# Kernel tuning notes

Hardware: AMD Instinct MI355X
Metric: run time of the kernel (lower is better)

## Reference

```python
import jax, jax.numpy as jnp
import numpy as np

N_NODES = 50000
N_EDGES = 800000
D_IN, D_HID, D_OUT = 64, 128, 64


def _glorot(key, fan_in, fan_out):
    lim = (6.0 / (fan_in + fan_out)) ** 0.5
    return jax.random.uniform(key, (fan_in, fan_out), jnp.float32, -lim, lim)


def setup_inputs() -> dict:
    key = jax.random.key(0)
    ks = jax.random.split(key, 10)
    x = jax.random.normal(ks[0], (N_NODES, D_IN), jnp.float32)
    edge_index = jax.random.randint(ks[1], (2, N_EDGES), 0, N_NODES, jnp.int64)
    # GINConv1 MLP: Linear(D_IN->D_HID), ReLU, Linear(D_HID->D_HID)
    W1a = _glorot(ks[2], D_IN, D_HID); b1a = jnp.zeros((D_HID,), jnp.float32)
    W1b = _glorot(ks[3], D_HID, D_HID); b1b = jnp.zeros((D_HID,), jnp.float32)
    # GINConv2 MLP: Linear(D_HID->D_HID), ReLU, Linear(D_HID->D_OUT)
    W2a = _glorot(ks[4], D_HID, D_HID); b2a = jnp.zeros((D_HID,), jnp.float32)
    W2b = _glorot(ks[5], D_HID, D_OUT); b2b = jnp.zeros((D_OUT,), jnp.float32)
    return {"x": x, "edge_index": edge_index,
            "W1a": W1a, "b1a": b1a, "W1b": W1b, "b1b": b1b,
            "W2a": W2a, "b2a": b2a, "W2b": W2b, "b2b": b2b}


def _gin_conv(x, src, dst, Wa, ba, Wb, bb):
    # GIN aggregation (eps = 0): h_i = x_i + sum_{j in N(i)} x_j
    msgs = x[src]                                   # [E, d] gather
    agg = jax.ops.segment_sum(msgs, dst, num_segments=x.shape[0])  # [N, d]
    h = x + agg
    # 2-layer MLP
    h = jax.nn.relu(h @ Wa + ba)
    return h @ Wb + bb


def reference(x, edge_index, W1a, b1a, W1b, b1b, W2a, b2a, W2b, b2b):
    src, dst = edge_index[0], edge_index[1]
    h = jax.nn.relu(_gin_conv(x, src, dst, W1a, b1a, W1b, b1b))
    h = jax.nn.relu(_gin_conv(h, src, dst, W2a, b2a, W2b, b2b))
    return h
```

## Files before the change

kernel.cpp:

```cpp
#include <hip/hip_runtime.h>

#define N_NODES 50000
#define N_EDGES 800000

typedef __attribute__((ext_vector_type(8))) short short8;
typedef __attribute__((ext_vector_type(4))) float floatx4;

static __device__ __forceinline__ unsigned short f2b(float f) {
    unsigned int u = __float_as_uint(f);
    unsigned int r = u + 0x7fffu + ((u >> 16) & 1u);
    return (unsigned short)(r >> 16);
}
static __device__ __forceinline__ unsigned int pk(float a, float b) {
    return (unsigned)f2b(a) | ((unsigned)f2b(b) << 16);
}
static __device__ __forceinline__ float blo(unsigned int u) {
    return __uint_as_float(u << 16);
}
static __device__ __forceinline__ float bhi(unsigned int u) {
    return __uint_as_float(u & 0xffff0000u);
}

static __device__ __forceinline__ void acc4(float* f, uint4 v0, uint4 v1,
                                            uint4 v2, uint4 v3) {
    f[0] += (blo(v0.x) + blo(v1.x)) + (blo(v2.x) + blo(v3.x));
    f[1] += (bhi(v0.x) + bhi(v1.x)) + (bhi(v2.x) + bhi(v3.x));
    f[2] += (blo(v0.y) + blo(v1.y)) + (blo(v2.y) + blo(v3.y));
    f[3] += (bhi(v0.y) + bhi(v1.y)) + (bhi(v2.y) + bhi(v3.y));
    f[4] += (blo(v0.z) + blo(v1.z)) + (blo(v2.z) + blo(v3.z));
    f[5] += (bhi(v0.z) + bhi(v1.z)) + (bhi(v2.z) + bhi(v3.z));
    f[6] += (blo(v0.w) + blo(v1.w)) + (blo(v2.w) + blo(v3.w));
    f[7] += (bhi(v0.w) + bhi(v1.w)) + (bhi(v2.w) + bhi(v3.w));
}

__global__ void hist_rank_kernel(const int* __restrict__ dst,
                                 int* __restrict__ deg, int* __restrict__ rank,
                                 int n) {
    int i = blockIdx.x * blockDim.x + threadIdx.x;
    if (i < n) rank[i] = atomicAdd(&deg[dst[i]], 1);
}

__global__ __launch_bounds__(1024) void scanA_kernel(
    const int* __restrict__ deg, int* __restrict__ bsum, int n) {
    __shared__ int s[1024];
    const int tid = threadIdx.x;
    int i = blockIdx.x * 1024 + tid;
    s[tid] = (i < n) ? ((deg[i] + 3) & ~3) : 0;
    __syncthreads();
    for (int d = 512; d > 0; d >>= 1) {
        if (tid < d) s[tid] += s[tid + d];
        __syncthreads();
    }
    if (tid == 0) bsum[blockIdx.x] = s[0];
}

__global__ __launch_bounds__(1024) void scanC_kernel(
    const int* __restrict__ deg, const int* __restrict__ bsum,
    int* __restrict__ off, int n) {
    __shared__ int s[1024];
    __shared__ int bpref;
    const int tid = threadIdx.x;
    if (tid == 0) {
        int p = 0;
        for (int j = 0; j < blockIdx.x; ++j) p += bsum[j];
        bpref = p;
    }
    const int i = blockIdx.x * 1024 + tid;
    const int v = (i < n) ? ((deg[i] + 3) & ~3) : 0;
    s[tid] = v;
    __syncthreads();
    for (int d = 1; d < 1024; d <<= 1) {
        int t = (tid >= d) ? s[tid - d] : 0;
        __syncthreads();
        s[tid] += t;
        __syncthreads();
    }
    const int excl = s[tid] - v + bpref;
    if (i < n) {
        off[i] = excl;
        if (i == n - 1) off[n] = excl + v;
    }
}

__global__ void fill_kernel(const int* __restrict__ src,
                            const int* __restrict__ dst,
                            const int* __restrict__ rank,
                            const int* __restrict__ off,
                            const int* __restrict__ deg,
                            unsigned short* __restrict__ nbr, int n,
                            int n_nodes) {
    int i = blockIdx.x * blockDim.x + threadIdx.x;
    if (i < n) {
        nbr[off[dst[i]] + rank[i]] = (unsigned short)src[i];
    } else if (i < n + n_nodes) {
        const int v = i - n;
        const int base = off[v];
        const int d = deg[v];
        const int pd = (d + 3) & ~3;
        for (int k = d; k < pd; ++k) nbr[base + k] = (unsigned short)N_NODES;
    }
}

__global__ __launch_bounds__(256) void prep_kernel(
    const float* __restrict__ W1a, const float* __restrict__ W1b,
    const float* __restrict__ W2a, const float* __restrict__ W2b,
    const float* __restrict__ x, unsigned short* __restrict__ W1aT,
    unsigned short* __restrict__ W1bT, unsigned short* __restrict__ W2aT,
    unsigned short* __restrict__ W2bT, unsigned short* __restrict__ xb,
    unsigned short* __restrict__ h, int* __restrict__ deg) {
    int i = blockIdx.x * 256 + threadIdx.x;
    if (i < 8192) {
        int n = i >> 6, k = i & 63;
        W1aT[i] = f2b(W1a[k * 128 + n]);
    } else if (i < 24576) {
        int j = i - 8192, n = j >> 7, k = j & 127;
        W1bT[j] = f2b(W1b[k * 128 + n]);
    } else if (i < 40960) {
        int j = i - 24576, n = j >> 7, k = j & 127;
        W2aT[j] = f2b(W2a[k * 128 + n]);
    } else if (i < 49152) {
        int j = i - 40960, n = j >> 7, k = j & 127;
        W2bT[j] = f2b(W2b[k * 64 + n]);
    } else if (i < 49152 + N_NODES * 16) {
        int j = i - 49152;
        float4 v = ((const float4*)x)[j];
        uint2 o;
        o.x = pk(v.x, v.y);
        o.y = pk(v.z, v.w);
        ((uint2*)xb)[j] = o;
    } else if (i < 49152 + N_NODES * 16 + N_NODES) {
        int j = i - (49152 + N_NODES * 16);
        deg[j] = 0;
    } else {
        int j = i - (49152 + N_NODES * 16 + N_NODES);
        uint4 z = {0u, 0u, 0u, 0u};
        if (j < 8)
            ((uint4*)(xb + (size_t)N_NODES * 64))[j] = z;
        else if (j < 24)
            ((uint4*)(h + (size_t)N_NODES * 128))[j - 8] = z;
    }
}

template <int DIN, int DH, int DOUT, bool OUT_BF16>
__global__ __launch_bounds__(256) void gin_fused_kernel(
    const unsigned short* __restrict__ xin, const int* __restrict__ off,
    const unsigned short* __restrict__ nbr,
    const unsigned short* __restrict__ WaT, const float* __restrict__ ba,
    const unsigned short* __restrict__ WbT, const float* __restrict__ bb,
    void* __restrict__ outp, int n_rows) {
    constexpr int LPR = DIN / 8;
    constexpr int ROWS = 256 / LPR;
    constexpr int SA = DIN + 16;
    constexpr int SH = DH + 16;
    __shared__ __attribute__((aligned(16))) unsigned short tA[ROWS * SA];
    __shared__ __attribute__((aligned(16))) unsigned short hidA[ROWS * SH];

    const int tid = threadIdx.x;
    const int row0 = blockIdx.x * ROWS;
    const int grp = tid / LPR;
    const int c = tid % LPR;
    const int node = row0 + grp;

    float f[8] = {0.f, 0.f, 0.f, 0.f, 0.f, 0.f, 0.f, 0.f};
    const uint4* xr = (const uint4*)xin;
    if (node < n_rows) {
        const uint4 a = xr[(size_t)node * LPR + c];
        f[0] = blo(a.x); f[1] = bhi(a.x);
        f[2] = blo(a.y); f[3] = bhi(a.y);
        f[4] = blo(a.z); f[5] = bhi(a.z);
        f[6] = blo(a.w); f[7] = bhi(a.w);
        const int lo = off[node], hi = off[node + 1];
        int j = lo;
        for (; j + 8 <= hi; j += 8) {
            const uint2 i0 = *(const uint2*)&nbr[j];
            const uint2 i1 = *(const uint2*)&nbr[j + 4];
            const int s0 = i0.x & 0xffff, s1 = i0.x >> 16;
            const int s2 = i0.y & 0xffff, s3 = i0.y >> 16;
            const int s4 = i1.x & 0xffff, s5 = i1.x >> 16;
            const int s6 = i1.y & 0xffff, s7 = i1.y >> 16;
            const uint4 v0 = xr[(size_t)s0 * LPR + c];
            const uint4 v1 = xr[(size_t)s1 * LPR + c];
            const uint4 v2 = xr[(size_t)s2 * LPR + c];
            const uint4 v3 = xr[(size_t)s3 * LPR + c];
            const uint4 v4 = xr[(size_t)s4 * LPR + c];
            const uint4 v5 = xr[(size_t)s5 * LPR + c];
            const uint4 v6 = xr[(size_t)s6 * LPR + c];
            const uint4 v7 = xr[(size_t)s7 * LPR + c];
            acc4(f, v0, v1, v2, v3);
            acc4(f, v4, v5, v6, v7);
        }
        if (j < hi) {
            const uint2 i0 = *(const uint2*)&nbr[j];
            const int s0 = i0.x & 0xffff, s1 = i0.x >> 16;
            const int s2 = i0.y & 0xffff, s3 = i0.y >> 16;
            const uint4 v0 = xr[(size_t)s0 * LPR + c];
            const uint4 v1 = xr[(size_t)s1 * LPR + c];
            const uint4 v2 = xr[(size_t)s2 * LPR + c];
            const uint4 v3 = xr[(size_t)s3 * LPR + c];
            acc4(f, v0, v1, v2, v3);
        }
    }
    uint4 o;
    o.x = pk(f[0], f[1]);
    o.y = pk(f[2], f[3]);
    o.z = pk(f[4], f[5]);
    o.w = pk(f[6], f[7]);
    *(uint4*)&tA[grp * SA + c * 8] = o;
    __syncthreads();

    constexpr int MT = ROWS / 16;
    constexpr int NSPLIT = 4 / MT;
    const int lane = tid & 63;
    const int wv = tid >> 6;
    const int wm = wv % MT;
    const int wn = wv / MT;
    const int quad = lane >> 4;
    const int l16 = lane & 15;
    const int m0 = wm * 16;

    short8 a1[DIN / 32];
#pragma unroll
    for (int kk = 0; kk < DIN / 32; ++kk)
        a1[kk] = *(const short8*)&tA[(m0 + l16) * SA + kk * 32 + quad * 8];
#pragma unroll
    for (int nt = 0; nt < DH / (16 * NSPLIT); ++nt) {
        const int col = wn * (DH / NSPLIT) + nt * 16 + l16;
        floatx4 acc = {0.f, 0.f, 0.f, 0.f};
#pragma unroll
        for (int kk = 0; kk < DIN / 32; ++kk) {
            short8 b = *(const short8*)&WaT[col * DIN + kk * 32 + quad * 8];
            acc = __builtin_amdgcn_mfma_f32_16x16x32_bf16(a1[kk], b, acc, 0, 0, 0);
        }
        const float bias = ba[col];
#pragma unroll
        for (int r = 0; r < 4; ++r) {
            const float v = fmaxf(acc[r] + bias, 0.f);
            hidA[(m0 + quad * 4 + r) * SH + col] = f2b(v);
        }
    }
    __syncthreads();

    short8 a2[DH / 32];
#pragma unroll
    for (int kk = 0; kk < DH / 32; ++kk)
        a2[kk] = *(const short8*)&hidA[(m0 + l16) * SH + kk * 32 + quad * 8];
#pragma unroll
    for (int nt = 0; nt < DOUT / (16 * NSPLIT); ++nt) {
        const int col = wn * (DOUT / NSPLIT) + nt * 16 + l16;
        floatx4 acc = {0.f, 0.f, 0.f, 0.f};
#pragma unroll
        for (int kk = 0; kk < DH / 32; ++kk) {
            short8 b = *(const short8*)&WbT[col * DH + kk * 32 + quad * 8];
            acc = __builtin_amdgcn_mfma_f32_16x16x32_bf16(a2[kk], b, acc, 0, 0, 0);
        }
        const float bias = bb[col];
#pragma unroll
        for (int r = 0; r < 4; ++r) {
            const float v = fmaxf(acc[r] + bias, 0.f);
            const int grow = row0 + m0 + quad * 4 + r;
            if (grow < n_rows) {
                if (OUT_BF16)
                    ((unsigned short*)outp)[(size_t)grow * DOUT + col] = f2b(v);
                else
                    ((float*)outp)[(size_t)grow * DOUT + col] = v;
            }
        }
    }
}

extern "C" void kernel_launch(void* const* d_in, const int* in_sizes, int n_in,
                              void* d_out, int out_size, void* d_ws,
                              size_t ws_size, hipStream_t stream) {
    const float* x   = (const float*)d_in[0];
    const int*   ei  = (const int*)d_in[1];
    const float* W1a = (const float*)d_in[2];
    const float* b1a = (const float*)d_in[3];
    const float* W1b = (const float*)d_in[4];
    const float* b1b = (const float*)d_in[5];
    const float* W2a = (const float*)d_in[6];
    const float* b2a = (const float*)d_in[7];
    const float* W2b = (const float*)d_in[8];
    const float* b2b = (const float*)d_in[9];
    float* out = (float*)d_out;

    const int* src = ei;
    const int* dst = ei + N_EDGES;

    unsigned short* xb = (unsigned short*)d_ws;
    unsigned short* h  = xb + (size_t)(N_NODES + 1) * 64;
    unsigned short* W1aT = h + (size_t)(N_NODES + 1) * 128;
    unsigned short* W1bT = W1aT + 8192;
    unsigned short* W2aT = W1bT + 16384;
    unsigned short* W2bT = W2aT + 16384;
    int* deg  = (int*)(W2bT + 8192);
    int* off  = deg + N_NODES;
    int* bsum = off + N_NODES + 1;
    int* rank = bsum + 64;
    unsigned short* nbr = (unsigned short*)(rank + N_EDGES);

    constexpr int NB = (N_NODES + 1023) / 1024;
    constexpr int PREP_THREADS = 49152 + N_NODES * 16 + N_NODES + 24;

    prep_kernel<<<(PREP_THREADS + 255) / 256, 256, 0, stream>>>(
        W1a, W1b, W2a, W2b, x, W1aT, W1bT, W2aT, W2bT, xb, h, deg);

    hist_rank_kernel<<<(N_EDGES + 255) / 256, 256, 0, stream>>>(dst, deg, rank,
                                                                N_EDGES);
    scanA_kernel<<<NB, 1024, 0, stream>>>(deg, bsum, N_NODES);
    scanC_kernel<<<NB, 1024, 0, stream>>>(deg, bsum, off, N_NODES);
    fill_kernel<<<(N_EDGES + N_NODES + 255) / 256, 256, 0, stream>>>(
        src, dst, rank, off, deg, nbr, N_EDGES, N_NODES);

    gin_fused_kernel<64, 128, 128, true>
        <<<(N_NODES + 31) / 32, 256, 0, stream>>>(xb, off, nbr, W1aT, b1a, W1bT,
                                                  b1b, h, N_NODES);

    gin_fused_kernel<128, 128, 64, false>
        <<<(N_NODES + 15) / 16, 256, 0, stream>>>(h, off, nbr, W2aT, b2a, W2bT,
                                                  b2b, out, N_NODES);
}
```

Before: 218.3 us.

## Sort nodes by in-degree so fused GIN blocks process balanced neighbor counts

Adds a degree histogram (an extra block in the scan-reduce kernel) and a counting-sort pass (extra blocks in the scan kernel) that builds a permutation of nodes ordered by clamped in-degree. Both fused GIN kernels then process rows in permuted order and scatter outputs back to the original node index. The aim is to cut intra-block and intra-wave load imbalance in the neighbor-gather loop. The cost is a serial single-block histogram, an extra indirection, scattered output writes, and less locality when reading each node's own row.

```diff
diff --git a/kernel.cpp b/kernel.cpp
--- a/kernel.cpp
+++ b/kernel.cpp
@@ -41,9 +41,34 @@
 }
 
 __global__ __launch_bounds__(1024) void scanA_kernel(
-    const int* __restrict__ deg, int* __restrict__ bsum, int n) {
+    const int* __restrict__ deg, int* __restrict__ bsum,
+    int* __restrict__ binoff, int n, int nb) {
+    const int tid = threadIdx.x;
+    if ((int)blockIdx.x == nb) {
+        __shared__ int bins[4][256];
+        ((int*)bins)[tid] = 0;
+        __syncthreads();
+        const int sub = (tid >> 6) & 3;
+        for (int i = tid; i < n; i += 1024) {
+            int d = deg[i];
+            d = d > 255 ? 255 : d;
+            atomicAdd(&bins[sub][d], 1);
+        }
+        __syncthreads();
+        if (tid < 256)
+            bins[0][tid] =
+                bins[0][tid] + bins[1][tid] + bins[2][tid] + bins[3][tid];
+        __syncthreads();
+        if (tid == 0) {
+            int run = 0;
+            for (int b = 0; b < 256; ++b) {
+                binoff[b] = run;
+                run += bins[0][b];
+            }
+        }
+        return;
+    }
     __shared__ int s[1024];
-    const int tid = threadIdx.x;
     int i = blockIdx.x * 1024 + tid;
     s[tid] = (i < n) ? ((deg[i] + 3) & ~3) : 0;
     __syncthreads();
@@ -56,13 +81,24 @@
 
 __global__ __launch_bounds__(1024) void scanC_kernel(
     const int* __restrict__ deg, const int* __restrict__ bsum,
-    int* __restrict__ off, int n) {
+    int* __restrict__ off, int* __restrict__ binoff, int* __restrict__ perm,
+    int n, int nb) {
+    const int tid = threadIdx.x;
+    if ((int)blockIdx.x >= nb) {
+        const int i = ((int)blockIdx.x - nb) * 1024 + tid;
+        if (i < n) {
+            int d = deg[i];
+            d = d > 255 ? 255 : d;
+            const int pos = atomicAdd(&binoff[d], 1);
+            perm[pos] = i;
+        }
+        return;
+    }
     __shared__ int s[1024];
     __shared__ int bpref;
-    const int tid = threadIdx.x;
     if (tid == 0) {
         int p = 0;
-        for (int j = 0; j < blockIdx.x; ++j) p += bsum[j];
+        for (int j = 0; j < (int)blockIdx.x; ++j) p += bsum[j];
         bpref = p;
     }
     const int i = blockIdx.x * 1024 + tid;
@@ -144,7 +180,7 @@
 template <int DIN, int DH, int DOUT, bool OUT_BF16>
 __global__ __launch_bounds__(256) void gin_fused_kernel(
     const unsigned short* __restrict__ xin, const int* __restrict__ off,
-    const unsigned short* __restrict__ nbr,
+    const unsigned short* __restrict__ nbr, const int* __restrict__ perm,
     const unsigned short* __restrict__ WaT, const float* __restrict__ ba,
     const unsigned short* __restrict__ WbT, const float* __restrict__ bb,
     void* __restrict__ outp, int n_rows) {
@@ -159,11 +195,12 @@
     const int row0 = blockIdx.x * ROWS;
     const int grp = tid / LPR;
     const int c = tid % LPR;
-    const int node = row0 + grp;
+    const int gnode = row0 + grp;
 
     float f[8] = {0.f, 0.f, 0.f, 0.f, 0.f, 0.f, 0.f, 0.f};
     const uint4* xr = (const uint4*)xin;
-    if (node < n_rows) {
+    if (gnode < n_rows) {
+        const int node = perm[gnode];
         const uint4 a = xr[(size_t)node * LPR + c];
         f[0] = blo(a.x); f[1] = bhi(a.x);
         f[2] = blo(a.y); f[3] = bhi(a.y);
@@ -257,12 +294,13 @@
 #pragma unroll
         for (int r = 0; r < 4; ++r) {
             const float v = fmaxf(acc[r] + bias, 0.f);
-            const int grow = row0 + m0 + quad * 4 + r;
-            if (grow < n_rows) {
+            const int gr = row0 + m0 + quad * 4 + r;
+            if (gr < n_rows) {
+                const int orow = perm[gr];
                 if (OUT_BF16)
-                    ((unsigned short*)outp)[(size_t)grow * DOUT + col] = f2b(v);
+                    ((unsigned short*)outp)[(size_t)orow * DOUT + col] = f2b(v);
                 else
-                    ((float*)outp)[(size_t)grow * DOUT + col] = v;
+                    ((float*)outp)[(size_t)orow * DOUT + col] = v;
             }
         }
     }
@@ -292,11 +330,13 @@
     unsigned short* W1bT = W1aT + 8192;
     unsigned short* W2aT = W1bT + 16384;
     unsigned short* W2bT = W2aT + 16384;
-    int* deg  = (int*)(W2bT + 8192);
-    int* off  = deg + N_NODES;
-    int* bsum = off + N_NODES + 1;
-    int* rank = bsum + 64;
-    unsigned short* nbr = (unsigned short*)(rank + N_EDGES);
+    int* deg    = (int*)(W2bT + 8192);
+    int* off    = deg + N_NODES;
+    int* bsum   = off + N_NODES + 1;
+    int* rank   = bsum + 64;
+    int* perm   = rank + N_EDGES;
+    int* binoff = perm + N_NODES;
+    unsigned short* nbr = (unsigned short*)(binoff + 256);
 
     constexpr int NB = (N_NODES + 1023) / 1024;
     constexpr int PREP_THREADS = 49152 + N_NODES * 16 + N_NODES + 24;
@@ -306,16 +346,17 @@
 
     hist_rank_kernel<<<(N_EDGES + 255) / 256, 256, 0, stream>>>(dst, deg, rank,
                                                                 N_EDGES);
-    scanA_kernel<<<NB, 1024, 0, stream>>>(deg, bsum, N_NODES);
-    scanC_kernel<<<NB, 1024, 0, stream>>>(deg, bsum, off, N_NODES);
+    scanA_kernel<<<NB + 1, 1024, 0, stream>>>(deg, bsum, binoff, N_NODES, NB);
+    scanC_kernel<<<2 * NB, 1024, 0, stream>>>(deg, bsum, off, binoff, perm,
+                                              N_NODES, NB);
     fill_kernel<<<(N_EDGES + N_NODES + 255) / 256, 256, 0, stream>>>(
         src, dst, rank, off, deg, nbr, N_EDGES, N_NODES);
 
     gin_fused_kernel<64, 128, 128, true>
-        <<<(N_NODES + 31) / 32, 256, 0, stream>>>(xb, off, nbr, W1aT, b1a, W1bT,
-                                                  b1b, h, N_NODES);
+        <<<(N_NODES + 31) / 32, 256, 0, stream>>>(xb, off, nbr, perm, W1aT, b1a,
+                                                  W1bT, b1b, h, N_NODES);
 
     gin_fused_kernel<128, 128, 64, false>
-        <<<(N_NODES + 15) / 16, 256, 0, stream>>>(h, off, nbr, W2aT, b2a, W2bT,
-                                                  b2b, out, N_NODES);
-}
+        <<<(N_NODES + 15) / 16, 256, 0, stream>>>(h, off, nbr, perm, W2aT, b2a,
+                                                  W2bT, b2b, out, N_NODES);
+}
```

Result: slower. 345.4 us (+58.2%).

## Sort rows by degree within block and unroll neighbor gather by 16

Applied to the files above, without the earlier changes.

Each block computes node degrees, ranks them in shared memory and assigns rows to thread groups in degree order, so lanes in the same wavefront handle nodes of similar degree and diverge less. Results are written back to their original row slot in shared memory. The main gather loop is unrolled to 16 neighbors per iteration to keep more loads in flight. This adds a small ranking pass with extra syncs and raises register pressure.

```diff
diff --git a/kernel.cpp b/kernel.cpp
--- a/kernel.cpp
+++ b/kernel.cpp
@@ -62,7 +62,7 @@
     const int tid = threadIdx.x;
     if (tid == 0) {
         int p = 0;
-        for (int j = 0; j < blockIdx.x; ++j) p += bsum[j];
+        for (int j = 0; j < (int)blockIdx.x; ++j) p += bsum[j];
         bpref = p;
     }
     const int i = blockIdx.x * 1024 + tid;
@@ -154,16 +154,38 @@
     constexpr int SH = DH + 16;
     __shared__ __attribute__((aligned(16))) unsigned short tA[ROWS * SA];
     __shared__ __attribute__((aligned(16))) unsigned short hidA[ROWS * SH];
+    __shared__ int sdeg[ROWS];
+    __shared__ int sperm[ROWS];
 
     const int tid = threadIdx.x;
     const int row0 = blockIdx.x * ROWS;
     const int grp = tid / LPR;
     const int c = tid % LPR;
-    const int node = row0 + grp;
+
+    if (tid < ROWS) {
+        const int nd = row0 + tid;
+        sdeg[tid] = (nd < n_rows) ? (off[nd + 1] - off[nd]) : 0;
+    }
+    __syncthreads();
+    if (tid < ROWS) {
+        const int d = sdeg[tid];
+        int rank = 0;
+#pragma unroll
+        for (int j = 0; j < ROWS; ++j) {
+            const int dj = sdeg[j];
+            rank += (dj < d) || (dj == d && j < tid);
+        }
+        sperm[rank] = tid;
+    }
+    __syncthreads();
+
+    const int lrow = sperm[grp];
+    const int gnode = row0 + lrow;
 
     float f[8] = {0.f, 0.f, 0.f, 0.f, 0.f, 0.f, 0.f, 0.f};
     const uint4* xr = (const uint4*)xin;
-    if (node < n_rows) {
+    if (gnode < n_rows) {
+        const int node = gnode;
         const uint4 a = xr[(size_t)node * LPR + c];
         f[0] = blo(a.x); f[1] = bhi(a.x);
         f[2] = blo(a.y); f[3] = bhi(a.y);
@@ -171,7 +193,41 @@
         f[6] = blo(a.w); f[7] = bhi(a.w);
         const int lo = off[node], hi = off[node + 1];
         int j = lo;
-        for (; j + 8 <= hi; j += 8) {
+        for (; j + 16 <= hi; j += 16) {
+            const uint2 i0 = *(const uint2*)&nbr[j];
+            const uint2 i1 = *(const uint2*)&nbr[j + 4];
+            const uint2 i2 = *(const uint2*)&nbr[j + 8];
+            const uint2 i3 = *(const uint2*)&nbr[j + 12];
+            const int s0 = i0.x & 0xffff, s1 = i0.x >> 16;
+            const int s2 = i0.y & 0xffff, s3 = i0.y >> 16;
+            const int s4 = i1.x & 0xffff, s5 = i1.x >> 16;
+            const int s6 = i1.y & 0xffff, s7 = i1.y >> 16;
+            const int s8 = i2.x & 0xffff, s9 = i2.x >> 16;
+            const int sa = i2.y & 0xffff, sb = i2.y >> 16;
+            const int sc = i3.x & 0xffff, sd = i3.x >> 16;
+            const int se = i3.y & 0xffff, sf = i3.y >> 16;
+            const uint4 v0 = xr[(size_t)s0 * LPR + c];
+            const uint4 v1 = xr[(size_t)s1 * LPR + c];
+            const uint4 v2 = xr[(size_t)s2 * LPR + c];
+            const uint4 v3 = xr[(size_t)s3 * LPR + c];
+            const uint4 v4 = xr[(size_t)s4 * LPR + c];
+            const uint4 v5 = xr[(size_t)s5 * LPR + c];
+            const uint4 v6 = xr[(size_t)s6 * LPR + c];
+            const uint4 v7 = xr[(size_t)s7 * LPR + c];
+            const uint4 v8 = xr[(size_t)s8 * LPR + c];
+            const uint4 v9 = xr[(size_t)s9 * LPR + c];
+            const uint4 va = xr[(size_t)sa * LPR + c];
+            const uint4 vb = xr[(size_t)sb * LPR + c];
+            const uint4 vc = xr[(size_t)sc * LPR + c];
+            const uint4 vd = xr[(size_t)sd * LPR + c];
+            const uint4 ve = xr[(size_t)se * LPR + c];
+            const uint4 vf = xr[(size_t)sf * LPR + c];
+            acc4(f, v0, v1, v2, v3);
+            acc4(f, v4, v5, v6, v7);
+            acc4(f, v8, v9, va, vb);
+            acc4(f, vc, vd, ve, vf);
+        }
+        if (j + 8 <= hi) {
             const uint2 i0 = *(const uint2*)&nbr[j];
             const uint2 i1 = *(const uint2*)&nbr[j + 4];
             const int s0 = i0.x & 0xffff, s1 = i0.x >> 16;
@@ -188,6 +244,7 @@
             const uint4 v7 = xr[(size_t)s7 * LPR + c];
             acc4(f, v0, v1, v2, v3);
             acc4(f, v4, v5, v6, v7);
+            j += 8;
         }
         if (j < hi) {
             const uint2 i0 = *(const uint2*)&nbr[j];
@@ -205,7 +262,7 @@
     o.y = pk(f[2], f[3]);
     o.z = pk(f[4], f[5]);
     o.w = pk(f[6], f[7]);
-    *(uint4*)&tA[grp * SA + c * 8] = o;
+    *(uint4*)&tA[lrow * SA + c * 8] = o;
     __syncthreads();
 
     constexpr int MT = ROWS / 16;
```

After: 231.9 us. +6.3%, slower.

## Replace two-pass scan with single atomic-offset kernel and packed offset/degree

Applied to the files above, without the earlier changes.

Merges the two scan kernels into one offsets kernel. Each block scans its padded degrees locally and claims a global base with an atomicAdd, so segment order across blocks no longer follows node order. Offset and padded degree are packed into one int (offset<<10 | pd), and the padding fill moves into this kernel, so the fill and GIN kernels read one word per node. This removes a launch and the serial per-block prefix loop, but it assumes padded degree stays below 1024 and offset below 2^21, and it makes the CSR layout depend on block scheduling order.

```diff
diff --git a/kernel.cpp b/kernel.cpp
--- a/kernel.cpp
+++ b/kernel.cpp
@@ -40,65 +40,39 @@
     if (i < n) rank[i] = atomicAdd(&deg[dst[i]], 1);
 }
 
-__global__ __launch_bounds__(1024) void scanA_kernel(
-    const int* __restrict__ deg, int* __restrict__ bsum, int n) {
+__global__ __launch_bounds__(1024) void offsets_kernel(
+    const int* __restrict__ deg, int* __restrict__ offpd,
+    int* __restrict__ gcount, unsigned short* __restrict__ nbr, int n) {
     __shared__ int s[1024];
+    __shared__ int base;
     const int tid = threadIdx.x;
-    int i = blockIdx.x * 1024 + tid;
-    s[tid] = (i < n) ? ((deg[i] + 3) & ~3) : 0;
-    __syncthreads();
-    for (int d = 512; d > 0; d >>= 1) {
-        if (tid < d) s[tid] += s[tid + d];
-        __syncthreads();
-    }
-    if (tid == 0) bsum[blockIdx.x] = s[0];
-}
-
-__global__ __launch_bounds__(1024) void scanC_kernel(
-    const int* __restrict__ deg, const int* __restrict__ bsum,
-    int* __restrict__ off, int n) {
-    __shared__ int s[1024];
-    __shared__ int bpref;
-    const int tid = threadIdx.x;
-    if (tid == 0) {
-        int p = 0;
-        for (int j = 0; j < blockIdx.x; ++j) p += bsum[j];
-        bpref = p;
-    }
     const int i = blockIdx.x * 1024 + tid;
-    const int v = (i < n) ? ((deg[i] + 3) & ~3) : 0;
-    s[tid] = v;
-    __syncthreads();
-    for (int d = 1; d < 1024; d <<= 1) {
-        int t = (tid >= d) ? s[tid - d] : 0;
+    const int d = (i < n) ? deg[i] : 0;
+    const int pd = (d + 3) & ~3;
+    s[tid] = pd;
+    __syncthreads();
+    for (int o = 1; o < 1024; o <<= 1) {
+        int t = (tid >= o) ? s[tid - o] : 0;
         __syncthreads();
         s[tid] += t;
         __syncthreads();
     }
-    const int excl = s[tid] - v + bpref;
+    if (tid == 1023) base = atomicAdd(gcount, s[1023]);
+    __syncthreads();
+    const int excl = base + s[tid] - pd;
     if (i < n) {
-        off[i] = excl;
-        if (i == n - 1) off[n] = excl + v;
+        offpd[i] = (excl << 10) | pd;
+        for (int k = d; k < pd; ++k) nbr[excl + k] = (unsigned short)N_NODES;
     }
 }
 
 __global__ void fill_kernel(const int* __restrict__ src,
                             const int* __restrict__ dst,
                             const int* __restrict__ rank,
-                            const int* __restrict__ off,
-                            const int* __restrict__ deg,
-                            unsigned short* __restrict__ nbr, int n,
-                            int n_nodes) {
+                            const int* __restrict__ offpd,
+                            unsigned short* __restrict__ nbr, int n) {
     int i = blockIdx.x * blockDim.x + threadIdx.x;
-    if (i < n) {
-        nbr[off[dst[i]] + rank[i]] = (unsigned short)src[i];
-    } else if (i < n + n_nodes) {
-        const int v = i - n;
-        const int base = off[v];
-        const int d = deg[v];
-        const int pd = (d + 3) & ~3;
-        for (int k = d; k < pd; ++k) nbr[base + k] = (unsigned short)N_NODES;
-    }
+    if (i < n) nbr[(offpd[dst[i]] >> 10) + rank[i]] = (unsigned short)src[i];
 }
 
 __global__ __launch_bounds__(256) void prep_kernel(
@@ -107,7 +81,8 @@
     const float* __restrict__ x, unsigned short* __restrict__ W1aT,
     unsigned short* __restrict__ W1bT, unsigned short* __restrict__ W2aT,
     unsigned short* __restrict__ W2bT, unsigned short* __restrict__ xb,
-    unsigned short* __restrict__ h, int* __restrict__ deg) {
+    unsigned short* __restrict__ h, int* __restrict__ deg,
+    int* __restrict__ gcount) {
     int i = blockIdx.x * 256 + threadIdx.x;
     if (i < 8192) {
         int n = i >> 6, k = i & 63;
@@ -131,6 +106,7 @@
     } else if (i < 49152 + N_NODES * 16 + N_NODES) {
         int j = i - (49152 + N_NODES * 16);
         deg[j] = 0;
+        if (j == 0) *gcount = 0;
     } else {
         int j = i - (49152 + N_NODES * 16 + N_NODES);
         uint4 z = {0u, 0u, 0u, 0u};
@@ -143,7 +119,7 @@
 
 template <int DIN, int DH, int DOUT, bool OUT_BF16>
 __global__ __launch_bounds__(256) void gin_fused_kernel(
-    const unsigned short* __restrict__ xin, const int* __restrict__ off,
+    const unsigned short* __restrict__ xin, const int* __restrict__ offpd,
     const unsigned short* __restrict__ nbr,
     const unsigned short* __restrict__ WaT, const float* __restrict__ ba,
     const unsigned short* __restrict__ WbT, const float* __restrict__ bb,
@@ -169,7 +145,9 @@
         f[2] = blo(a.y); f[3] = bhi(a.y);
         f[4] = blo(a.z); f[5] = bhi(a.z);
         f[6] = blo(a.w); f[7] = bhi(a.w);
-        const int lo = off[node], hi = off[node + 1];
+        const int v = offpd[node];
+        const int lo = v >> 10;
+        const int hi = lo + (v & 1023);
         int j = lo;
         for (; j + 8 <= hi; j += 8) {
             const uint2 i0 = *(const uint2*)&nbr[j];
@@ -292,30 +270,29 @@
     unsigned short* W1bT = W1aT + 8192;
     unsigned short* W2aT = W1bT + 16384;
     unsigned short* W2bT = W2aT + 16384;
-    int* deg  = (int*)(W2bT + 8192);
-    int* off  = deg + N_NODES;
-    int* bsum = off + N_NODES + 1;
-    int* rank = bsum + 64;
+    int* deg    = (int*)(W2bT + 8192);
+    int* offpd  = deg + N_NODES;
+    int* gcount = offpd + N_NODES;
+    int* rank   = gcount + 64;
     unsigned short* nbr = (unsigned short*)(rank + N_EDGES);
 
     constexpr int NB = (N_NODES + 1023) / 1024;
     constexpr int PREP_THREADS = 49152 + N_NODES * 16 + N_NODES + 24;
 
     prep_kernel<<<(PREP_THREADS + 255) / 256, 256, 0, stream>>>(
-        W1a, W1b, W2a, W2b, x, W1aT, W1bT, W2aT, W2bT, xb, h, deg);
+        W1a, W1b, W2a, W2b, x, W1aT, W1bT, W2aT, W2bT, xb, h, deg, gcount);
 
     hist_rank_kernel<<<(N_EDGES + 255) / 256, 256, 0, stream>>>(dst, deg, rank,
                                                                 N_EDGES);
-    scanA_kernel<<<NB, 1024, 0, stream>>>(deg, bsum, N_NODES);
-    scanC_kernel<<<NB, 1024, 0, stream>>>(deg, bsum, off, N_NODES);
-    fill_kernel<<<(N_EDGES + N_NODES + 255) / 256, 256, 0, stream>>>(
-        src, dst, rank, off, deg, nbr, N_EDGES, N_NODES);
+    offsets_kernel<<<NB, 1024, 0, stream>>>(deg, offpd, gcount, nbr, N_NODES);
+    fill_kernel<<<(N_EDGES + 255) / 256, 256, 0, stream>>>(src, dst, rank,
+                                                           offpd, nbr, N_EDGES);
 
     gin_fused_kernel<64, 128, 128, true>
-        <<<(N_NODES + 31) / 32, 256, 0, stream>>>(xb, off, nbr, W1aT, b1a, W1bT,
-                                                  b1b, h, N_NODES);
+        <<<(N_NODES + 31) / 32, 256, 0, stream>>>(xb, offpd, nbr, W1aT, b1a,
+                                                  W1bT, b1b, h, N_NODES);
 
     gin_fused_kernel<128, 128, 64, false>
-        <<<(N_NODES + 15) / 16, 256, 0, stream>>>(h, off, nbr, W2aT, b2a, W2bT,
-                                                  b2b, out, N_NODES);
-}
+        <<<(N_NODES + 15) / 16, 256, 0, stream>>>(h, offpd, nbr, W2aT, b2a,
+                                                  W2bT, b2b, out, N_NODES);
+}
```

New measurement: 217.3 us, median of 2. No clear change (-0.5%).
